# Kernel optimization log

Hardware: AMD Instinct MI355X
Metric: run time of the kernel (lower is better)

## Reference

```python
import jax, jax.numpy as jnp
import numpy as np

KS = 3        # kernel_size
DIL = 2       # dilation
HEAD_DIM = 32


def _unfold(x, ks, dil):
    """torch nn.Unfold(ks, dilation=dil, padding=dil*(ks-1)//2, stride=1).
    x: [B, C, H, W] -> [B, C, ks*ks, H, W] (channel-major patch order, matching torch)."""
    B, C, H, W = x.shape
    pad = dil * (ks - 1) // 2
    xp = jnp.pad(x, ((0, 0), (0, 0), (pad, pad), (pad, pad)))
    pats = [xp[:, :, i * dil:i * dil + H, j * dil:j * dil + W]
            for i in range(ks) for j in range(ks)]
    return jnp.stack(pats, axis=2)


def setup_inputs() -> dict:
    key = jax.random.key(0)
    k1, k2, k3 = jax.random.split(key, 3)
    shape = (16, 128, 64, 64)  # [B, d, H, W]
    return {
        "q": jax.random.normal(k1, shape, dtype=jnp.float32),
        "k": jax.random.normal(k2, shape, dtype=jnp.float32),
        "v": jax.random.normal(k3, shape, dtype=jnp.float32),
    }


def reference(q, k, v):
    B, d, H, W = q.shape
    heads = d // HEAD_DIM
    scale = HEAD_DIM ** (-0.5)
    KK = KS * KS
    # q: [B, heads, head_dim, H*W]
    qr = q.reshape(B, heads, HEAD_DIM, H * W)
    # unfolded k/v: [B, heads, head_dim, KK, H*W]
    ku = _unfold(k, KS, DIL).reshape(B, heads, HEAD_DIM, KK, H * W)
    vu = _unfold(v, KS, DIL).reshape(B, heads, HEAD_DIM, KK, H * W)
    # per-pixel small attention over KK local dilated keys
    attn = jnp.einsum('bhdn,bhdkn->bhnk', qr, ku) * scale  # [B,heads,HW,KK]
    attn = jax.nn.softmax(attn, axis=-1)  # attn_drop = 0 -> identity
    out = jnp.einsum('bhnk,bhdkn->bnhd', attn, vu)  # [B,HW,heads,head_dim]
    return out.reshape(B, H, W, d)
```

## Files before the change

### kernel.cpp

```cpp
#include <hip/hip_runtime.h>

namespace {
constexpr float SCALE = 0.17677669529663687f;
constexpr int CHP = 256;

typedef const __attribute__((address_space(1))) void gbl_v;
typedef __attribute__((address_space(3))) void lds_v;

__global__ __launch_bounds__(512, 4) void dilate_attn(
    const float* __restrict__ q, const float* __restrict__ k,
    const float* __restrict__ v, float* __restrict__ out) {
  __shared__ float kbuf[32 * CHP];
  __shared__ float vbuf[32 * CHP];

  const int tid = threadIdx.x;
  const int cg  = tid & 7;
  const int pp  = (tid >> 3) & 31;
  const int rg  = tid >> 8;

  const int blk   = blockIdx.x;
  const int s     = blk >> 3;
  const int combo = ((blk & 7) << 3) | (s >> 5);
  const int pr    = s & 31;
  const int r0    = ((pr >> 1) << 2) | (pr & 1);
  const int b     = combo >> 2;
  const int head  = combo & 3;
  const int qrow  = r0 + 2 * rg;

  const size_t cb = ((size_t)b * 128 + head * 32) * 4096;
  const float* kp = k + cb;
  const float* vp = v + cb;

  int srow[4]; float vm[4];
  #pragma unroll
  for (int j = 0; j < 4; ++j) {
    const int ry = r0 - 2 + 2 * j;
    const bool ok = (unsigned)ry < 64u;
    srow[j] = (ok ? ry : r0) * 64;
    vm[j]   = ok ? 1.0f : 0.0f;
  }

  const int px0 = pp << 1;
  float2 q2[4];
  #pragma unroll
  for (int ci = 0; ci < 4; ++ci) {
    q2[ci] = *(const float2*)(q + cb + (cg * 4 + ci) * 4096 + qrow * 64 + px0);
    q2[ci].x *= SCALE;
    q2[ci].y *= SCALE;
  }

  #pragma unroll
  for (int t = 0; t < 4; ++t) {
    const int l4  = t * 512 + tid;
    const int ch  = l4 >> 6;
    const int rem = l4 & 63;
    const int r   = rem >> 4;
    const int q4  = rem & 15;
    const int pxs = ((q4 - (ch >> 2)) & 15) << 2;
    const int go  = ch * 4096 + srow[r] + pxs;
    const int lo  = l4 << 2;
    __builtin_amdgcn_global_load_lds((gbl_v*)(kp + go), (lds_v*)(kbuf + lo), 16, 0, 0);
    __builtin_amdgcn_global_load_lds((gbl_v*)(vp + go), (lds_v*)(vbuf + lo), 16, 0, 0);
  }

  __syncthreads();

  const int   txL = (pp == 0)  ? 0  : px0 - 2;
  const int   txC = px0;
  const int   txR = (pp == 31) ? 62 : px0 + 2;
  const float mL  = (pp == 0)  ? 0.0f : 1.0f;
  const float mR  = (pp == 31) ? 0.0f : 1.0f;

  const int rot = cg << 2;
  const int tL  = (txL + rot) & 63;
  const int tC  = (txC + rot) & 63;
  const int tR  = (txR + rot) & 63;

  const int rbase = rg;

  float l0[9], l1[9];
  #pragma unroll
  for (int t = 0; t < 9; ++t) { l0[t] = 0.0f; l1[t] = 0.0f; }

  #pragma unroll
  for (int r = 0; r < 3; ++r) {
    #pragma unroll
    for (int ci = 0; ci < 4; ++ci) {
      const float* kc = kbuf + (cg * 4 + ci) * CHP + (rbase + r) * 64;
      const float2 kL = *(const float2*)(kc + tL);
      const float2 kC = *(const float2*)(kc + tC);
      const float2 kR = *(const float2*)(kc + tR);
      const float2 qq = q2[ci];
      l0[r*3+0] = fmaf(qq.x, kL.x, l0[r*3+0]);
      l1[r*3+0] = fmaf(qq.y, kL.y, l1[r*3+0]);
      l0[r*3+1] = fmaf(qq.x, kC.x, l0[r*3+1]);
      l1[r*3+1] = fmaf(qq.y, kC.y, l1[r*3+1]);
      l0[r*3+2] = fmaf(qq.x, kR.x, l0[r*3+2]);
      l1[r*3+2] = fmaf(qq.y, kR.y, l1[r*3+2]);
    }
  }

  #pragma unroll
  for (int m = 1; m <= 4; m <<= 1) {
    #pragma unroll
    for (int t = 0; t < 9; ++t) {
      l0[t] += __shfl_xor(l0[t], m, 64);
      l1[t] += __shfl_xor(l1[t], m, 64);
    }
  }

  float msk[9];
  #pragma unroll
  for (int r = 0; r < 3; ++r) {
    msk[r*3+0] = vm[rbase + r] * mL;
    msk[r*3+1] = vm[rbase + r];
    msk[r*3+2] = vm[rbase + r] * mR;
  }
  float s0 = 0.0f, s1 = 0.0f;
  #pragma unroll
  for (int t = 0; t < 9; ++t) {
    l0[t] = __expf(l0[t] * msk[t]);
    l1[t] = __expf(l1[t] * msk[t]);
    s0 += l0[t]; s1 += l1[t];
  }
  const float r0v = 1.0f / s0, r1v = 1.0f / s1;
  #pragma unroll
  for (int t = 0; t < 9; ++t) {
    l0[t] *= r0v * msk[t];
    l1[t] *= r1v * msk[t];
  }

  float o0[4] = {0, 0, 0, 0}, o1[4] = {0, 0, 0, 0};
  #pragma unroll
  for (int r = 0; r < 3; ++r) {
    #pragma unroll
    for (int ci = 0; ci < 4; ++ci) {
      const float* vc = vbuf + (cg * 4 + ci) * CHP + (rbase + r) * 64;
      const float2 vL = *(const float2*)(vc + tL);
      const float2 vC = *(const float2*)(vc + tC);
      const float2 vR = *(const float2*)(vc + tR);
      o0[ci] = fmaf(l0[r*3+0], vL.x, o0[ci]);
      o0[ci] = fmaf(l0[r*3+1], vC.x, o0[ci]);
      o0[ci] = fmaf(l0[r*3+2], vR.x, o0[ci]);
      o1[ci] = fmaf(l1[r*3+0], vL.y, o1[ci]);
      o1[ci] = fmaf(l1[r*3+1], vC.y, o1[ci]);
      o1[ci] = fmaf(l1[r*3+2], vR.y, o1[ci]);
    }
  }

  float* ob = out + ((size_t)(b * 64 + qrow) * 64 + px0) * 128 + head * 32 + cg * 4;
  *(float4*)(ob)       = make_float4(o0[0], o0[1], o0[2], o0[3]);
  *(float4*)(ob + 128) = make_float4(o1[0], o1[1], o1[2], o1[3]);
}
}

extern "C" void kernel_launch(void* const* d_in, const int* in_sizes, int n_in,
                              void* d_out, int out_size, void* d_ws, size_t ws_size,
                              hipStream_t stream) {
  const float* q = (const float*)d_in[0];
  const float* k = (const float*)d_in[1];
  const float* v = (const float*)d_in[2];
  float* o = (float*)d_out;
  dilate_attn<<<dim3(2048), dim3(512), 0, stream>>>(q, k, v, o);
}
```

Measured before the change: 139.4 us.

## Split K/V LDS loads with partial waitcnt barriers and use packed float2 FMAs

All K global-to-LDS loads are issued before the V loads. The first barrier now waits only for the K loads (vmcnt(4)), so the QK logits and softmax run while V is still in flight, and a second barrier waits for V before the PV accumulation. The math is also rewritten with two-wide vector types so the compiler can emit packed FMA/mul instructions (v_pk_fma_f32) for the two pixels per thread. The hand-written waitcnt depends on exact instruction ordering, and the extra barrier adds synchronisation cost.

```diff
diff --git a/kernel.cpp b/kernel.cpp
--- a/kernel.cpp
+++ b/kernel.cpp
@@ -6,6 +6,7 @@
 
 typedef const __attribute__((address_space(1))) void gbl_v;
 typedef __attribute__((address_space(3))) void lds_v;
+typedef float v2f __attribute__((ext_vector_type(2)));
 
 __global__ __launch_bounds__(512, 4) void dilate_attn(
     const float* __restrict__ q, const float* __restrict__ k,
@@ -41,14 +42,14 @@
   }
 
   const int px0 = pp << 1;
-  float2 q2[4];
+  v2f q2[4];
   #pragma unroll
   for (int ci = 0; ci < 4; ++ci) {
-    q2[ci] = *(const float2*)(q + cb + (cg * 4 + ci) * 4096 + qrow * 64 + px0);
-    q2[ci].x *= SCALE;
-    q2[ci].y *= SCALE;
+    q2[ci] = *(const v2f*)(q + cb + (cg * 4 + ci) * 4096 + qrow * 64 + px0);
+    q2[ci] *= SCALE;
   }
 
+  int goff[4], loff[4];
   #pragma unroll
   for (int t = 0; t < 4; ++t) {
     const int l4  = t * 512 + tid;
@@ -57,13 +58,19 @@
     const int r   = rem >> 4;
     const int q4  = rem & 15;
     const int pxs = ((q4 - (ch >> 2)) & 15) << 2;
-    const int go  = ch * 4096 + srow[r] + pxs;
-    const int lo  = l4 << 2;
-    __builtin_amdgcn_global_load_lds((gbl_v*)(kp + go), (lds_v*)(kbuf + lo), 16, 0, 0);
-    __builtin_amdgcn_global_load_lds((gbl_v*)(vp + go), (lds_v*)(vbuf + lo), 16, 0, 0);
+    goff[t] = ch * 4096 + srow[r] + pxs;
+    loff[t] = l4 << 2;
   }
+  #pragma unroll
+  for (int t = 0; t < 4; ++t)
+    __builtin_amdgcn_global_load_lds((gbl_v*)(kp + goff[t]), (lds_v*)(kbuf + loff[t]), 16, 0, 0);
+  #pragma unroll
+  for (int t = 0; t < 4; ++t)
+    __builtin_amdgcn_global_load_lds((gbl_v*)(vp + goff[t]), (lds_v*)(vbuf + loff[t]), 16, 0, 0);
 
-  __syncthreads();
+  asm volatile("s_waitcnt vmcnt(4)" ::: "memory");
+  __builtin_amdgcn_s_barrier();
+  asm volatile("" ::: "memory");
 
   const int   txL = (pp == 0)  ? 0  : px0 - 2;
   const int   txC = px0;
@@ -78,25 +85,21 @@
 
   const int rbase = rg;
 
-  float l0[9], l1[9];
+  v2f l[9];
   #pragma unroll
-  for (int t = 0; t < 9; ++t) { l0[t] = 0.0f; l1[t] = 0.0f; }
+  for (int t = 0; t < 9; ++t) l[t] = (v2f)(0.0f);
 
   #pragma unroll
   for (int r = 0; r < 3; ++r) {
     #pragma unroll
     for (int ci = 0; ci < 4; ++ci) {
       const float* kc = kbuf + (cg * 4 + ci) * CHP + (rbase + r) * 64;
-      const float2 kL = *(const float2*)(kc + tL);
-      const float2 kC = *(const float2*)(kc + tC);
-      const float2 kR = *(const float2*)(kc + tR);
-      const float2 qq = q2[ci];
-      l0[r*3+0] = fmaf(qq.x, kL.x, l0[r*3+0]);
-      l1[r*3+0] = fmaf(qq.y, kL.y, l1[r*3+0]);
-      l0[r*3+1] = fmaf(qq.x, kC.x, l0[r*3+1]);
-      l1[r*3+1] = fmaf(qq.y, kC.y, l1[r*3+1]);
-      l0[r*3+2] = fmaf(qq.x, kR.x, l0[r*3+2]);
-      l1[r*3+2] = fmaf(qq.y, kR.y, l1[r*3+2]);
+      const v2f kL = *(const v2f*)(kc + tL);
+      const v2f kC = *(const v2f*)(kc + tC);
+      const v2f kR = *(const v2f*)(kc + tR);
+      l[r*3+0] = __builtin_elementwise_fma(q2[ci], kL, l[r*3+0]);
+      l[r*3+1] = __builtin_elementwise_fma(q2[ci], kC, l[r*3+1]);
+      l[r*3+2] = __builtin_elementwise_fma(q2[ci], kR, l[r*3+2]);
     }
   }
 
@@ -104,8 +107,10 @@
   for (int m = 1; m <= 4; m <<= 1) {
     #pragma unroll
     for (int t = 0; t < 9; ++t) {
-      l0[t] += __shfl_xor(l0[t], m, 64);
-      l1[t] += __shfl_xor(l1[t], m, 64);
+      v2f tmp;
+      tmp.x = __shfl_xor(l[t].x, m, 64);
+      tmp.y = __shfl_xor(l[t].y, m, 64);
+      l[t] += tmp;
     }
   }
 
@@ -116,41 +121,43 @@
     msk[r*3+1] = vm[rbase + r];
     msk[r*3+2] = vm[rbase + r] * mR;
   }
-  float s0 = 0.0f, s1 = 0.0f;
+  v2f sum = (v2f)(0.0f);
   #pragma unroll
   for (int t = 0; t < 9; ++t) {
-    l0[t] = __expf(l0[t] * msk[t]);
-    l1[t] = __expf(l1[t] * msk[t]);
-    s0 += l0[t]; s1 += l1[t];
+    l[t] *= msk[t];
+    l[t].x = __expf(l[t].x);
+    l[t].y = __expf(l[t].y);
+    sum += l[t];
   }
-  const float r0v = 1.0f / s0, r1v = 1.0f / s1;
+  v2f rv; rv.x = 1.0f / sum.x; rv.y = 1.0f / sum.y;
   #pragma unroll
-  for (int t = 0; t < 9; ++t) {
-    l0[t] *= r0v * msk[t];
-    l1[t] *= r1v * msk[t];
-  }
+  for (int t = 0; t < 9; ++t)
+    l[t] *= rv * msk[t];
 
-  float o0[4] = {0, 0, 0, 0}, o1[4] = {0, 0, 0, 0};
+  asm volatile("s_waitcnt vmcnt(0)" ::: "memory");
+  __builtin_amdgcn_s_barrier();
+  asm volatile("" ::: "memory");
+
+  v2f o[4];
+  #pragma unroll
+  for (int ci = 0; ci < 4; ++ci) o[ci] = (v2f)(0.0f);
   #pragma unroll
   for (int r = 0; r < 3; ++r) {
     #pragma unroll
     for (int ci = 0; ci < 4; ++ci) {
       const float* vc = vbuf + (cg * 4 + ci) * CHP + (rbase + r) * 64;
-      const float2 vL = *(const float2*)(vc + tL);
-      const float2 vC = *(const float2*)(vc + tC);
-      const float2 vR = *(const float2*)(vc + tR);
-      o0[ci] = fmaf(l0[r*3+0], vL.x, o0[ci]);
-      o0[ci] = fmaf(l0[r*3+1], vC.x, o0[ci]);
-      o0[ci] = fmaf(l0[r*3+2], vR.x, o0[ci]);
-      o1[ci] = fmaf(l1[r*3+0], vL.y, o1[ci]);
-      o1[ci] = fmaf(l1[r*3+1], vC.y, o1[ci]);
-      o1[ci] = fmaf(l1[r*3+2], vR.y, o1[ci]);
+      const v2f vL = *(const v2f*)(vc + tL);
+      const v2f vC = *(const v2f*)(vc + tC);
+      const v2f vR = *(const v2f*)(vc + tR);
+      o[ci] = __builtin_elementwise_fma(l[r*3+0], vL, o[ci]);
+      o[ci] = __builtin_elementwise_fma(l[r*3+1], vC, o[ci]);
+      o[ci] = __builtin_elementwise_fma(l[r*3+2], vR, o[ci]);
     }
   }
 
   float* ob = out + ((size_t)(b * 64 + qrow) * 64 + px0) * 128 + head * 32 + cg * 4;
-  *(float4*)(ob)       = make_float4(o0[0], o0[1], o0[2], o0[3]);
-  *(float4*)(ob + 128) = make_float4(o1[0], o1[1], o1[2], o1[3]);
+  *(float4*)(ob)       = make_float4(o[0].x, o[1].x, o[2].x, o[3].x);
+  *(float4*)(ob + 128) = make_float4(o[0].y, o[1].y, o[2].y, o[3].y);
 }
 }
 
```

After: 140.2 us. About the same (+0.6%).
